# Performance work log

Hardware: AMD Instinct MI355X
Metric: run time of the kernel (lower is better)

Reference implementation:

```python
import jax, jax.numpy as jnp
import numpy as np

B, C3, T = 32, 384, 2048

def setup_inputs() -> dict:
    key = jax.random.key(0)
    qkv = jax.random.normal(key, (B, C3, T), dtype=jnp.float32)
    return {"qkv": qkv}

def reference(qkv):
    # qkv: [B, 3C, T]
    ch = qkv.shape[1] // 3
    q, k, v = jnp.split(qkv, 3, axis=1)  # each [B, C, T]
    scale = 1.0 / jnp.sqrt(jnp.asarray(ch, dtype=qkv.dtype))
    # weight[b, t_q, t_k] = sum_c q[b,c,t_q] * k[b,c,t_k]
    weight = jnp.einsum('bcq,bck->bqk', q, k) * scale  # [B, T, T]
    weight = jax.nn.softmax(weight, axis=-1)
    # out[b, c, t_q] = sum_k weight[b,t_q,k] * v[b,c,k]
    out = jnp.einsum('bqk,bck->bcq', weight, v)  # [B, C, T]
    return out
```

## Files before the change

### kernel.cpp

```cpp
#include <hip/hip_runtime.h>
#include <hip/hip_bf16.h>
#include <math.h>

#define BB 32
#define CC 128
#define TT 2048
#define NCH 384

typedef __attribute__((ext_vector_type(8))) short short8;
typedef __attribute__((ext_vector_type(4))) float floatx4;

__device__ ushort g_q[(size_t)BB * TT * CC];
__device__ ushort g_k[(size_t)BB * TT * CC];
__device__ ushort g_v[(size_t)BB * CC * TT];

__device__ __forceinline__ ushort f2bf(float f) {
    uint u = __float_as_uint(f);
    u += 0x7fffu + ((u >> 16) & 1u);
    return (ushort)(u >> 16);
}

__global__ __launch_bounds__(256) void prepass_kernel(const float* __restrict__ qkv) {
    __shared__ float lds[64][132];
    const int b = blockIdx.y;
    const int t0 = blockIdx.x * 64;
    const int tid = threadIdx.x;

    for (int part = 0; part < 2; ++part) {
        const int c = tid >> 1;
        const int tb = (tid & 1) * 32;
        const float* src = qkv + ((size_t)(b * NCH + part * CC + c)) * TT + t0 + tb;
#pragma unroll
        for (int k = 0; k < 8; k++) {
            float4 f = *(const float4*)(src + 4 * k);
            lds[tb + 4 * k + 0][c] = f.x;
            lds[tb + 4 * k + 1][c] = f.y;
            lds[tb + 4 * k + 2][c] = f.z;
            lds[tb + 4 * k + 3][c] = f.w;
        }
        __syncthreads();
        const float scale = (part == 0) ? 0.08838834764831845f : 1.0f;
        ushort* dst = (part == 0 ? g_q : g_k) + ((size_t)(b * TT + t0)) * CC;
#pragma unroll
        for (int p = 0; p < 4; p++) {
            int t = p * 16 + (tid >> 4);
            int x = tid & 15;
            int cb = x ^ (t & 7);
            ushort tmp[8];
#pragma unroll
            for (int j = 0; j < 8; j++) tmp[j] = f2bf(lds[t][cb * 8 + j] * scale);
            *(uint4*)(dst + (size_t)t * CC + x * 8) = *(uint4*)tmp;
        }
        __syncthreads();
    }
    {
        const int c = tid >> 1;
        const int tb = (tid & 1) * 32;
        const float* src = qkv + ((size_t)(b * NCH + 2 * CC + c)) * TT + t0 + tb;
        ushort* dst = g_v + ((size_t)(b * CC + c)) * TT + t0;
#pragma unroll
        for (int k = 0; k < 8; k++) {
            float4 f = *(const float4*)(src + 4 * k);
            int tt = tb + 4 * k;
            int blk = tt >> 3;
            int off = tt & 7;
            int dblk = blk ^ (c & 7);
            ushort tmp[4] = {f2bf(f.x), f2bf(f.y), f2bf(f.z), f2bf(f.w)};
            *(uint2*)(dst + dblk * 8 + off) = *(uint2*)tmp;
        }
    }
}

__global__ __launch_bounds__(256) void attn_kernel(float* __restrict__ out) {
    __shared__ ushort Qs[64][128];
    __shared__ ushort Ks[64][128];
    __shared__ ushort Vs[128][64];
    __shared__ ushort Ps[4][16][72];

    const int b = blockIdx.y;
    const int q0 = blockIdx.x * 64;
    const int tid = threadIdx.x;
    const int w = tid >> 6;
    const int l = tid & 63;
    const int g = l >> 4;
    const int ln = l & 15;

    {
        const uint4* src = (const uint4*)(g_q + ((size_t)(b * TT + q0)) * CC);
        uint4* d = (uint4*)&Qs[0][0];
#pragma unroll
        for (int i = 0; i < 4; i++) d[i * 256 + tid] = src[i * 256 + tid];
    }

    floatx4 oacc[8];
#pragma unroll
    for (int i = 0; i < 8; i++) oacc[i] = (floatx4){0.f, 0.f, 0.f, 0.f};
    float m_run = -INFINITY;
    float l_run = 0.f;

    const int qt_loc = (w << 4) | ln;
    const int qswz = qt_loc & 7;

    for (int kt0 = 0; kt0 < TT; kt0 += 64) {
        __syncthreads();
        {
            const uint4* src = (const uint4*)(g_k + ((size_t)(b * TT + kt0)) * CC);
            uint4* d = (uint4*)&Ks[0][0];
#pragma unroll
            for (int i = 0; i < 4; i++) d[i * 256 + tid] = src[i * 256 + tid];
        }
        {
            const ushort* src = g_v + ((size_t)(b * CC)) * TT + kt0;
            uint4* d = (uint4*)&Vs[0][0];
#pragma unroll
            for (int i = 0; i < 4; i++) {
                int idx = i * 256 + tid;
                int c = idx >> 3, o = idx & 7;
                d[idx] = *(const uint4*)(src + (size_t)c * TT + o * 8);
            }
        }
        __syncthreads();

        floatx4 sacc[4];
#pragma unroll
        for (int s = 0; s < 4; s++) sacc[s] = (floatx4){0.f, 0.f, 0.f, 0.f};
#pragma unroll
        for (int ck = 0; ck < 4; ck++) {
            int cbq = (4 * ck + g) ^ qswz;
            short8 bq = *(const short8*)&Qs[qt_loc][cbq * 8];
#pragma unroll
            for (int s = 0; s < 4; s++) {
                int kt = 16 * s + ln;
                int cbk = (4 * ck + g) ^ (kt & 7);
                short8 ak = *(const short8*)&Ks[kt][cbk * 8];
                sacc[s] = __builtin_amdgcn_mfma_f32_16x16x32_bf16(ak, bq, sacc[s], 0, 0, 0);
            }
        }

        float vmax = -INFINITY;
#pragma unroll
        for (int s = 0; s < 4; s++)
            vmax = fmaxf(vmax, fmaxf(fmaxf(sacc[s].x, sacc[s].y), fmaxf(sacc[s].z, sacc[s].w)));
        vmax = fmaxf(vmax, __shfl_xor(vmax, 16));
        vmax = fmaxf(vmax, __shfl_xor(vmax, 32));
        float mnew = fmaxf(m_run, vmax);
        float alpha = __expf(m_run - mnew);
        float rs = 0.f;
#pragma unroll
        for (int s = 0; s < 4; s++) {
            float p0 = __expf(sacc[s].x - mnew);
            float p1 = __expf(sacc[s].y - mnew);
            float p2 = __expf(sacc[s].z - mnew);
            float p3 = __expf(sacc[s].w - mnew);
            rs += (p0 + p1) + (p2 + p3);
            uint lo = (uint)f2bf(p0) | ((uint)f2bf(p1) << 16);
            uint hi = (uint)f2bf(p2) | ((uint)f2bf(p3) << 16);
            *(uint*)&Ps[w][ln][16 * s + 4 * g] = lo;
            *(uint*)&Ps[w][ln][16 * s + 4 * g + 2] = hi;
        }
        rs += __shfl_xor(rs, 16);
        rs += __shfl_xor(rs, 32);
        l_run = l_run * alpha + rs;
        m_run = mnew;
#pragma unroll
        for (int i = 0; i < 8; i++) {
            oacc[i].x *= alpha; oacc[i].y *= alpha;
            oacc[i].z *= alpha; oacc[i].w *= alpha;
        }

#pragma unroll
        for (int kk = 0; kk < 2; kk++) {
            short8 bp = *(const short8*)&Ps[w][ln][32 * kk + 8 * g];
#pragma unroll
            for (int ms = 0; ms < 8; ms++) {
                int c = 16 * ms + ln;
                int y = (4 * kk + g) ^ (c & 7);
                short8 av = *(const short8*)&Vs[c][y * 8];
                oacc[ms] = __builtin_amdgcn_mfma_f32_16x16x32_bf16(av, bp, oacc[ms], 0, 0, 0);
            }
        }
    }

    float inv = 1.0f / l_run;
    float* op = out + ((size_t)(b * CC)) * TT + q0 + qt_loc;
#pragma unroll
    for (int ms = 0; ms < 8; ms++) {
#pragma unroll
        for (int r = 0; r < 4; r++) {
            int c = 16 * ms + 4 * g + r;
            op[(size_t)c * TT] = oacc[ms][r] * inv;
        }
    }
}

extern "C" void kernel_launch(void* const* d_in, const int* in_sizes, int n_in,
                              void* d_out, int out_size, void* d_ws, size_t ws_size,
                              hipStream_t stream) {
    (void)in_sizes; (void)n_in; (void)d_ws; (void)ws_size; (void)out_size;
    const float* qkv = (const float*)d_in[0];
    float* out = (float*)d_out;
    dim3 grid(32, 32), blk(256);
    hipLaunchKernelGGL(prepass_kernel, grid, blk, 0, stream, qkv);
    hipLaunchKernelGGL(attn_kernel, grid, blk, 0, stream, out);
}
```

Measured before the change: 308.3 us.

## Hold Q in registers, use exp2 with lazy rescale, and coalesce prepass loads

The attention kernel now keeps the Q fragments in registers and reuses the Q LDS buffer for the P tile. The Q prescale is folded into log2(e)/sqrt(C) so softmax can use exp2f. The running-max rescale is skipped while the new max stays within 8 of the old one, which removes most of the alpha multiplies on the accumulators. The prepass reorganises its global loads for better coalescing, pads the LDS tile to reduce bank conflicts, and writes V as 16-byte stores. The lazy rescale allows probabilities up to 2^8 before normalisation, which costs some bf16 precision headroom.

```diff
diff --git a/kernel.cpp b/kernel.cpp
--- a/kernel.cpp
+++ b/kernel.cpp
@@ -21,25 +21,35 @@
 }
 
 __global__ __launch_bounds__(256) void prepass_kernel(const float* __restrict__ qkv) {
-    __shared__ float lds[64][132];
+    __shared__ float lds[64][133];
     const int b = blockIdx.y;
     const int t0 = blockIdx.x * 64;
     const int tid = threadIdx.x;
+    const int u = tid >> 3;
+    const int j = tid & 7;
 
     for (int part = 0; part < 2; ++part) {
-        const int c = tid >> 1;
-        const int tb = (tid & 1) * 32;
-        const float* src = qkv + ((size_t)(b * NCH + part * CC + c)) * TT + t0 + tb;
-#pragma unroll
-        for (int k = 0; k < 8; k++) {
-            float4 f = *(const float4*)(src + 4 * k);
-            lds[tb + 4 * k + 0][c] = f.x;
-            lds[tb + 4 * k + 1][c] = f.y;
-            lds[tb + 4 * k + 2][c] = f.z;
-            lds[tb + 4 * k + 3][c] = f.w;
+        const float scale = (part == 0) ? 0.127517451f : 1.0f;
+        float4 fa[4][2];
+#pragma unroll
+        for (int i = 0; i < 4; i++) {
+            const float* src = qkv + ((size_t)(b * NCH + part * CC + i * 32 + u)) * TT + t0 + j * 8;
+            fa[i][0] = *(const float4*)src;
+            fa[i][1] = *(const float4*)(src + 4);
+        }
+        if (part) __syncthreads();
+#pragma unroll
+        for (int i = 0; i < 4; i++) {
+            int c = i * 32 + u;
+#pragma unroll
+            for (int q = 0; q < 2; q++) {
+                lds[j * 8 + q * 4 + 0][c] = fa[i][q].x;
+                lds[j * 8 + q * 4 + 1][c] = fa[i][q].y;
+                lds[j * 8 + q * 4 + 2][c] = fa[i][q].z;
+                lds[j * 8 + q * 4 + 3][c] = fa[i][q].w;
+            }
         }
         __syncthreads();
-        const float scale = (part == 0) ? 0.08838834764831845f : 1.0f;
         ushort* dst = (part == 0 ? g_q : g_k) + ((size_t)(b * TT + t0)) * CC;
 #pragma unroll
         for (int p = 0; p < 4; p++) {
@@ -48,25 +58,23 @@
             int cb = x ^ (t & 7);
             ushort tmp[8];
 #pragma unroll
-            for (int j = 0; j < 8; j++) tmp[j] = f2bf(lds[t][cb * 8 + j] * scale);
+            for (int jj = 0; jj < 8; jj++) tmp[jj] = f2bf(lds[t][cb * 8 + jj] * scale);
             *(uint4*)(dst + (size_t)t * CC + x * 8) = *(uint4*)tmp;
         }
-        __syncthreads();
     }
     {
-        const int c = tid >> 1;
-        const int tb = (tid & 1) * 32;
-        const float* src = qkv + ((size_t)(b * NCH + 2 * CC + c)) * TT + t0 + tb;
-        ushort* dst = g_v + ((size_t)(b * CC + c)) * TT + t0;
-#pragma unroll
-        for (int k = 0; k < 8; k++) {
-            float4 f = *(const float4*)(src + 4 * k);
-            int tt = tb + 4 * k;
-            int blk = tt >> 3;
-            int off = tt & 7;
-            int dblk = blk ^ (c & 7);
-            ushort tmp[4] = {f2bf(f.x), f2bf(f.y), f2bf(f.z), f2bf(f.w)};
-            *(uint2*)(dst + dblk * 8 + off) = *(uint2*)tmp;
+        const float* vsrc = qkv + ((size_t)(b * NCH + 2 * CC)) * TT + t0;
+        ushort* vdst = g_v + ((size_t)(b * CC)) * TT + t0;
+#pragma unroll
+        for (int i = 0; i < 4; i++) {
+            int idx = i * 256 + tid;
+            int c = idx >> 3, db = idx & 7, sb = db ^ (c & 7);
+            const float* s = vsrc + (size_t)c * TT + sb * 8;
+            float4 f0 = *(const float4*)s;
+            float4 f1 = *(const float4*)(s + 4);
+            ushort tmp[8] = {f2bf(f0.x), f2bf(f0.y), f2bf(f0.z), f2bf(f0.w),
+                             f2bf(f1.x), f2bf(f1.y), f2bf(f1.z), f2bf(f1.w)};
+            *(uint4*)(vdst + (size_t)c * TT + db * 8) = *(uint4*)tmp;
         }
     }
 }
@@ -75,7 +83,7 @@
     __shared__ ushort Qs[64][128];
     __shared__ ushort Ks[64][128];
     __shared__ ushort Vs[128][64];
-    __shared__ ushort Ps[4][16][72];
+    ushort (*Ps)[16][72] = reinterpret_cast<ushort(*)[16][72]>(&Qs[0][0]);
 
     const int b = blockIdx.y;
     const int q0 = blockIdx.x * 64;
@@ -84,6 +92,8 @@
     const int l = tid & 63;
     const int g = l >> 4;
     const int ln = l & 15;
+    const int qt_loc = (w << 4) | ln;
+    const int qswz = qt_loc & 7;
 
     {
         const uint4* src = (const uint4*)(g_q + ((size_t)(b * TT + q0)) * CC);
@@ -91,15 +101,19 @@
 #pragma unroll
         for (int i = 0; i < 4; i++) d[i * 256 + tid] = src[i * 256 + tid];
     }
+    __syncthreads();
+    short8 qfrag[4];
+#pragma unroll
+    for (int ck = 0; ck < 4; ck++) {
+        int cbq = (4 * ck + g) ^ qswz;
+        qfrag[ck] = *(const short8*)&Qs[qt_loc][cbq * 8];
+    }
 
     floatx4 oacc[8];
 #pragma unroll
     for (int i = 0; i < 8; i++) oacc[i] = (floatx4){0.f, 0.f, 0.f, 0.f};
     float m_run = -INFINITY;
     float l_run = 0.f;
-
-    const int qt_loc = (w << 4) | ln;
-    const int qswz = qt_loc & 7;
 
     for (int kt0 = 0; kt0 < TT; kt0 += 64) {
         __syncthreads();
@@ -126,14 +140,12 @@
         for (int s = 0; s < 4; s++) sacc[s] = (floatx4){0.f, 0.f, 0.f, 0.f};
 #pragma unroll
         for (int ck = 0; ck < 4; ck++) {
-            int cbq = (4 * ck + g) ^ qswz;
-            short8 bq = *(const short8*)&Qs[qt_loc][cbq * 8];
 #pragma unroll
             for (int s = 0; s < 4; s++) {
                 int kt = 16 * s + ln;
                 int cbk = (4 * ck + g) ^ (kt & 7);
                 short8 ak = *(const short8*)&Ks[kt][cbk * 8];
-                sacc[s] = __builtin_amdgcn_mfma_f32_16x16x32_bf16(ak, bq, sacc[s], 0, 0, 0);
+                sacc[s] = __builtin_amdgcn_mfma_f32_16x16x32_bf16(ak, qfrag[ck], sacc[s], 0, 0, 0);
             }
         }
 
@@ -143,30 +155,33 @@
             vmax = fmaxf(vmax, fmaxf(fmaxf(sacc[s].x, sacc[s].y), fmaxf(sacc[s].z, sacc[s].w)));
         vmax = fmaxf(vmax, __shfl_xor(vmax, 16));
         vmax = fmaxf(vmax, __shfl_xor(vmax, 32));
-        float mnew = fmaxf(m_run, vmax);
-        float alpha = __expf(m_run - mnew);
+        if (!__all(vmax <= m_run + 8.0f)) {
+            float mnew = fmaxf(m_run, vmax);
+            float alpha = exp2f(m_run - mnew);
+            l_run *= alpha;
+#pragma unroll
+            for (int i = 0; i < 8; i++) {
+                oacc[i].x *= alpha; oacc[i].y *= alpha;
+                oacc[i].z *= alpha; oacc[i].w *= alpha;
+            }
+            m_run = mnew;
+        }
         float rs = 0.f;
 #pragma unroll
         for (int s = 0; s < 4; s++) {
-            float p0 = __expf(sacc[s].x - mnew);
-            float p1 = __expf(sacc[s].y - mnew);
-            float p2 = __expf(sacc[s].z - mnew);
-            float p3 = __expf(sacc[s].w - mnew);
+            float p0 = exp2f(sacc[s].x - m_run);
+            float p1 = exp2f(sacc[s].y - m_run);
+            float p2 = exp2f(sacc[s].z - m_run);
+            float p3 = exp2f(sacc[s].w - m_run);
             rs += (p0 + p1) + (p2 + p3);
-            uint lo = (uint)f2bf(p0) | ((uint)f2bf(p1) << 16);
-            uint hi = (uint)f2bf(p2) | ((uint)f2bf(p3) << 16);
-            *(uint*)&Ps[w][ln][16 * s + 4 * g] = lo;
-            *(uint*)&Ps[w][ln][16 * s + 4 * g + 2] = hi;
+            __hip_bfloat162 lo = __float22bfloat162_rn(make_float2(p0, p1));
+            __hip_bfloat162 hi = __float22bfloat162_rn(make_float2(p2, p3));
+            *(__hip_bfloat162*)&Ps[w][ln][16 * s + 4 * g] = lo;
+            *(__hip_bfloat162*)&Ps[w][ln][16 * s + 4 * g + 2] = hi;
         }
         rs += __shfl_xor(rs, 16);
         rs += __shfl_xor(rs, 32);
-        l_run = l_run * alpha + rs;
-        m_run = mnew;
-#pragma unroll
-        for (int i = 0; i < 8; i++) {
-            oacc[i].x *= alpha; oacc[i].y *= alpha;
-            oacc[i].z *= alpha; oacc[i].w *= alpha;
-        }
+        l_run += rs;
 
 #pragma unroll
         for (int kk = 0; kk < 2; kk++) {
```

Result: no change. 302.6 us (-1.8%).
